# Performance work log

Measured on AMD Instinct MI355X. Metric: run time of the kernel, lower is better.

Reference implementation:

```python
import jax, jax.numpy as jnp
import numpy as np


def setup_inputs() -> dict:
    key = jax.random.key(0)
    ks = jax.random.split(key, 8)
    B, C, H, W = 8, 64, 256, 256
    Cq = C // 8
    return {
        "x": jax.random.normal(ks[0], (B, C, H, W), dtype=jnp.float32),
        "Wq": jax.random.normal(ks[1], (Cq, C), dtype=jnp.float32) * 0.1,
        "bq": jax.random.normal(ks[2], (Cq,), dtype=jnp.float32) * 0.1,
        "Wk": jax.random.normal(ks[3], (Cq, C), dtype=jnp.float32) * 0.1,
        "bk": jax.random.normal(ks[4], (Cq,), dtype=jnp.float32) * 0.1,
        "Wv": jax.random.normal(ks[5], (C, C), dtype=jnp.float32) * 0.1,
        "bv": jax.random.normal(ks[6], (C,), dtype=jnp.float32) * 0.1,
        "gamma": jax.random.normal(ks[7], (1,), dtype=jnp.float32),
    }


def _criss_cross(x, Wq, bq, Wk, bk, Wv, bv, gamma):
    # 1x1 convs == per-pixel linear maps over channel dim
    q = jnp.einsum('bchw,oc->bohw', x, Wq) + bq[None, :, None, None]  # [B,Cq,H,W]
    k = jnp.einsum('bchw,oc->bohw', x, Wk) + bk[None, :, None, None]  # [B,Cq,H,W]
    v = jnp.einsum('bchw,oc->bohw', x, Wv) + bv[None, :, None, None]  # [B,C,H,W]

    # --- column (height) attention: independent per (b, w) ---
    # attn_h[b,w,i,j] = <q[:, :, i, w], k[:, :, j, w]>, softmax over j
    attn_h = jnp.einsum('bciw,bcjw->bwij', q, k)            # [B,W,H,H]
    attn_h = jax.nn.softmax(attn_h, axis=-1)
    # torch: h_out = bmm(value[BW,C,H], attn[BW,H,H]) -> out[c,j] = sum_i v[c,i]*attn[i,j]
    h_out = jnp.einsum('bciw,bwij->bcjw', v, attn_h)        # [B,C,H,W]

    # --- row (width) attention: independent per (b, h) ---
    attn_w = jnp.einsum('bchw,bchv->bhwv', q, k)            # [B,H,W,W]
    attn_w = jax.nn.softmax(attn_w, axis=-1)
    w_out = jnp.einsum('bchw,bhwv->bchv', v, attn_w)        # [B,C,H,W]

    return gamma[0] * (h_out + w_out) + x


def reference(x, Wq, bq, Wk, bk, Wv, bv, gamma):
    return _criss_cross(x, Wq, bq, Wk, bk, Wv, bv, gamma)
```

## Files before the change

kernel.cpp:

```cpp
#include <hip/hip_runtime.h>
#include <cstddef>

namespace {

constexpr int    Bn   = 8;
constexpr int    Cc   = 64;
constexpr int    Cq   = 8;
constexpr int    Ln   = 256;
constexpr size_t HWn  = 65536;
constexpr size_t NPIX = (size_t)Bn * HWn;
constexpr size_t VPLANE = NPIX * 16;

constexpr float LOG2E = 1.44269504088896f;

constexpr size_t WT_B = 0;
constexpr size_t QH_B = 32768;
constexpr size_t QL_B = QH_B + NPIX * 8 * 2;
constexpr size_t KH_B = QL_B + NPIX * 8 * 2;
constexpr size_t KL_B = KH_B + NPIX * 8 * 2;
constexpr size_t VB_B = KL_B + NPIX * 8 * 2;
constexpr size_t HO_B = VB_B + NPIX * 64 * 2;

typedef short bf16x8 __attribute__((ext_vector_type(8)));
typedef float f32x16 __attribute__((ext_vector_type(16)));
typedef unsigned short u16x4 __attribute__((ext_vector_type(4)));

__device__ __forceinline__ unsigned short f2bf(float x) {
  union { float f; unsigned u; } c; c.f = x;
  unsigned u = c.u + 0x7FFFu + ((c.u >> 16) & 1u);
  return (unsigned short)(u >> 16);
}
__device__ __forceinline__ float bf2f(unsigned short h) {
  union { unsigned u; float f; } c; c.u = ((unsigned)h) << 16;
  return c.f;
}
__device__ __forceinline__ float fast_exp2(float x) {
#if __has_builtin(__builtin_amdgcn_exp2f)
  return __builtin_amdgcn_exp2f(x);
#else
  float r;
  asm("v_exp_f32 %0, %1" : "=v"(r) : "v"(x));
  return r;
#endif
}
__device__ __forceinline__ f32x16 zero16() {
  f32x16 z;
#pragma unroll
  for (int i = 0; i < 16; ++i) z[i] = 0.f;
  return z;
}

}

__global__ void pack_weights(const float* __restrict__ Wq,
                             const float* __restrict__ Wk,
                             const float* __restrict__ Wv,
                             float* __restrict__ wt) {
  int idx = blockIdx.x * 256 + threadIdx.x;
  if (idx >= 64 * 80) return;
  int c = idx / 80, o = idx % 80;
  float v;
  if (o < 8)       v = Wq[o * 64 + c] * LOG2E;
  else if (o < 16) v = Wk[(o - 8) * 64 + c];
  else             v = Wv[(o - 16) * 64 + c];
  wt[idx] = v;
}

__global__ __launch_bounds__(256) void qkv_kernel(
    const float* __restrict__ x, const float* __restrict__ wt,
    const float* __restrict__ bq, const float* __restrict__ bk,
    const float* __restrict__ bv,
    unsigned short* __restrict__ qh, unsigned short* __restrict__ ql,
    unsigned short* __restrict__ kh, unsigned short* __restrict__ kl,
    unsigned short* __restrict__ vb) {
  const int chunk = blockIdx.x;
  size_t p = (size_t)blockIdx.y * 256 + threadIdx.x;
  int b = (int)(p >> 16);
  int rem = (int)(p & 65535);
  const float* xb = x + (size_t)b * 64 * HWn + rem;

  float acc[16];
  if (chunk == 0) {
#pragma unroll
    for (int o = 0; o < 8; ++o) { acc[o] = bq[o] * LOG2E; acc[8 + o] = bk[o]; }
  } else {
#pragma unroll
    for (int o = 0; o < 16; ++o) acc[o] = bv[(chunk - 1) * 16 + o];
  }
  const int woff = (chunk == 0) ? 0 : 16 + (chunk - 1) * 16;

#pragma unroll 1
  for (int c0 = 0; c0 < 64; c0 += 8) {
    float xv[8];
#pragma unroll
    for (int cc = 0; cc < 8; ++cc) xv[cc] = xb[(size_t)(c0 + cc) * HWn];
#pragma unroll
    for (int cc = 0; cc < 8; ++cc) {
      const float* w = wt + (c0 + cc) * 80 + woff;
      const float xc = xv[cc];
#pragma unroll
      for (int o = 0; o < 16; ++o) acc[o] = fmaf(xc, w[o], acc[o]);
    }
  }

  if (chunk == 0) {
    unsigned h8[16], l8[16];
#pragma unroll
    for (int o = 0; o < 16; ++o) {
      h8[o] = f2bf(acc[o]);
      l8[o] = f2bf(acc[o] - bf2f((unsigned short)h8[o]));
    }
    uint4 pqh = make_uint4(h8[0] | (h8[1] << 16), h8[2] | (h8[3] << 16),
                           h8[4] | (h8[5] << 16), h8[6] | (h8[7] << 16));
    uint4 pql = make_uint4(l8[0] | (l8[1] << 16), l8[2] | (l8[3] << 16),
                           l8[4] | (l8[5] << 16), l8[6] | (l8[7] << 16));
    uint4 pkh = make_uint4(h8[8] | (h8[9] << 16), h8[10] | (h8[11] << 16),
                           h8[12] | (h8[13] << 16), h8[14] | (h8[15] << 16));
    uint4 pkl = make_uint4(l8[8] | (l8[9] << 16), l8[10] | (l8[11] << 16),
                           l8[12] | (l8[13] << 16), l8[14] | (l8[15] << 16));
    *(uint4*)(qh + p * 8) = pqh;
    *(uint4*)(ql + p * 8) = pql;
    *(uint4*)(kh + p * 8) = pkh;
    *(uint4*)(kl + p * 8) = pkl;
  } else {
    unsigned e[16];
#pragma unroll
    for (int u = 0; u < 16; ++u) e[u] = f2bf(acc[u]);
    uint4 p0 = make_uint4(e[0] | (e[1] << 16), e[2] | (e[3] << 16),
                          e[4] | (e[5] << 16), e[6] | (e[7] << 16));
    uint4 p1 = make_uint4(e[8] | (e[9] << 16), e[10] | (e[11] << 16),
                          e[12] | (e[13] << 16), e[14] | (e[15] << 16));
    unsigned short* vp = vb + (size_t)(chunk - 1) * VPLANE + p * 16;
    *(uint4*)(vp + 0) = p0;
    *(uint4*)(vp + 8) = p1;
  }
}

template <int MODE>
__global__ __launch_bounds__(256) void attn_kernel(
    const unsigned short* __restrict__ qh, const unsigned short* __restrict__ ql,
    const unsigned short* __restrict__ kh, const unsigned short* __restrict__ kl,
    const unsigned short* __restrict__ vb, float* __restrict__ o) {
  const int s = (MODE == 1) ? (((blockIdx.x & 7) << 8) | (blockIdx.x >> 3))
                            : blockIdx.x;
  const int t = threadIdx.x;
  const int b = s >> 8;
  const int r = s & 255;
  const int w = t >> 6;
  const int l = t & 63;
  const int g = l >> 5;
  const int ln = l & 31;

  __shared__ short qs_h[256 * 8], qs_l[256 * 8];
  __shared__ short ks_h[256 * 8], ks_l[256 * 8];
  __shared__ short vz[16384];
  __shared__ float Zl[256];

  size_t qkb, qk_stride;
  size_t v_pix_base, v_pix_stride;
  if (MODE == 0) {
    qkb    = (size_t)s * (Ln * Cq);  qk_stride = Cq;
    v_pix_base = (size_t)s * Ln;     v_pix_stride = 1;
  } else {
    qkb    = ((size_t)b * HWn + r) * Cq;  qk_stride = (size_t)Ln * Cq;
    v_pix_base = (size_t)b * HWn + r;     v_pix_stride = Ln;
  }

  {
    const size_t off = qkb + (size_t)t * qk_stride;
    *(bf16x8*)&qs_h[t * 8] = *(const bf16x8*)(qh + off);
    *(bf16x8*)&qs_l[t * 8] = *(const bf16x8*)(ql + off);
    *(bf16x8*)&ks_h[t * 8] = *(const bf16x8*)(kh + off);
    *(bf16x8*)&ks_l[t * 8] = *(const bf16x8*)(kl + off);
  }
  Zl[t] = 0.f;
  __syncthreads();

  {
    const short* kb = g ? ks_l : ks_h;
    bf16x8 afk0 = *(const bf16x8*)&kb[(ln + 32 * (2 * w + 0)) * 8];
    bf16x8 afk1 = *(const bf16x8*)&kb[(ln + 32 * (2 * w + 1)) * 8];
#pragma unroll 1
    for (int it = 0; it < 8; ++it) {
      int i = ln + 32 * it;
      bf16x8 bh = *(const bf16x8*)&qs_h[i * 8];
      bf16x8 bl = *(const bf16x8*)&qs_l[i * 8];
      float zp = 0.f;
      {
        f32x16 c = zero16();
        c = __builtin_amdgcn_mfma_f32_32x32x16_bf16(afk0, bh, c, 0, 0, 0);
        c = __builtin_amdgcn_mfma_f32_32x32x16_bf16(afk0, bl, c, 0, 0, 0);
#pragma unroll
        for (int rr = 0; rr < 16; ++rr) zp += fast_exp2(c[rr]);
      }
      {
        f32x16 c = zero16();
        c = __builtin_amdgcn_mfma_f32_32x32x16_bf16(afk1, bh, c, 0, 0, 0);
        c = __builtin_amdgcn_mfma_f32_32x32x16_bf16(afk1, bl, c, 0, 0, 0);
#pragma unroll
        for (int rr = 0; rr < 16; ++rr) zp += fast_exp2(c[rr]);
      }
      atomicAdd(&Zl[i], zp);
    }
  }
  __syncthreads();
  Zl[t] = 1.0f / Zl[t];
  __syncthreads();

#pragma unroll 1
  for (int rnd = 0; rnd < 16; ++rnd) {
    int idx = rnd * 256 + t;
    int i = idx >> 4;
    int c4 = (idx & 15) << 2;
    const unsigned short* vp = vb + (size_t)(c4 >> 4) * VPLANE +
                               (v_pix_base + (size_t)i * v_pix_stride) * 16 +
                               (c4 & 15);
    u16x4 raw = *(const u16x4*)vp;
    float iz = Zl[i];
    int sg = i >> 4, rem = i & 15;
    int a = rem >> 3, g2 = (rem >> 2) & 1, t0 = rem & 3;
    int e = 4 * a + t0;
#pragma unroll
    for (int u = 0; u < 4; ++u) {
      int c = c4 + u;
      int lane_s = 32 * g2 + (c & 31);
      int mt = c >> 5;
      vz[((sg * 2 + mt) * 64 + lane_s) * 8 + e] =
          (short)f2bf(bf2f(raw[u]) * iz);
    }
  }
  __syncthreads();

  f32x16 acc00 = zero16(), acc01 = zero16(), acc10 = zero16(), acc11 = zero16();
  {
    bf16x8 bkh[2], bkl[2];
#pragma unroll
    for (int nt2 = 0; nt2 < 2; ++nt2) {
      int j = ln + 32 * (2 * w + nt2);
      bkh[nt2] = *(const bf16x8*)&ks_h[j * 8];
      bkl[nt2] = *(const bf16x8*)&ks_l[j * 8];
    }
    const short* qb = g ? qs_l : qs_h;
#pragma unroll 1
    for (int it = 0; it < 8; ++it) {
      int i = ln + 32 * it;
      bf16x8 aQ = *(const bf16x8*)&qb[i * 8];
      bf16x8 pf[2][2];
#pragma unroll
      for (int nt2 = 0; nt2 < 2; ++nt2) {
        f32x16 c = zero16();
        c = __builtin_amdgcn_mfma_f32_32x32x16_bf16(aQ, bkh[nt2], c, 0, 0, 0);
        c = __builtin_amdgcn_mfma_f32_32x32x16_bf16(aQ, bkl[nt2], c, 0, 0, 0);
#pragma unroll
        for (int rr = 0; rr < 8; ++rr)
          pf[nt2][0][rr] = (short)f2bf(fast_exp2(c[rr]));
#pragma unroll
        for (int rr = 0; rr < 8; ++rr)
          pf[nt2][1][rr] = (short)f2bf(fast_exp2(c[8 + rr]));
      }
#pragma unroll
      for (int s2 = 0; s2 < 2; ++s2) {
#pragma unroll
        for (int mt = 0; mt < 2; ++mt) {
          bf16x8 vf = *(const bf16x8*)&vz[(((it * 2 + s2) * 2 + mt) * 64 + l) * 8];
          if (mt == 0) {
            acc00 = __builtin_amdgcn_mfma_f32_32x32x16_bf16(vf, pf[0][s2], acc00, 0, 0, 0);
            acc10 = __builtin_amdgcn_mfma_f32_32x32x16_bf16(vf, pf[1][s2], acc10, 0, 0, 0);
          } else {
            acc01 = __builtin_amdgcn_mfma_f32_32x32x16_bf16(vf, pf[0][s2], acc01, 0, 0, 0);
            acc11 = __builtin_amdgcn_mfma_f32_32x32x16_bf16(vf, pf[1][s2], acc11, 0, 0, 0);
          }
        }
      }
    }
  }

#pragma unroll
  for (int nt2 = 0; nt2 < 2; ++nt2) {
    int j = ln + 32 * (2 * w + nt2);
#pragma unroll
    for (int mt = 0; mt < 2; ++mt) {
      const f32x16& A = (nt2 == 0) ? (mt == 0 ? acc00 : acc01)
                                   : (mt == 0 ? acc10 : acc11);
#pragma unroll
      for (int reg = 0; reg < 16; ++reg) {
        int c = (reg & 3) + 8 * (reg >> 2) + 4 * g + 32 * mt;
        if (MODE == 0) {
          o[((size_t)b * 64 + c) * HWn + (size_t)r * 256 + j] = A[reg];
        } else {
          o[((size_t)s * 64 + c) * 256 + j] = A[reg];
        }
      }
    }
  }
}

__global__ __launch_bounds__(256) void merge_kernel(
    const float* __restrict__ wout, const float* __restrict__ ho,
    const float* __restrict__ x, const float* __restrict__ gamma,
    float* __restrict__ out) {
  const int h0 = blockIdx.x * 32;
  const int c = blockIdx.y;
  const int b = blockIdx.z;
  const int t = threadIdx.x;
  __shared__ float lds[256 * 33];

  const float g = gamma[0];

#pragma unroll
  for (int it = 0; it < 8; ++it) {
    int e = it * 256 + t;
    int w = e >> 3, q4 = (e & 7) << 2;
    float4 f = *(const float4*)&ho[(((size_t)b * 256 + w) * 64 + c) * 256 + h0 + q4];
    lds[w * 33 + q4 + 0] = f.x;
    lds[w * 33 + q4 + 1] = f.y;
    lds[w * 33 + q4 + 2] = f.z;
    lds[w * 33 + q4 + 3] = f.w;
  }
  __syncthreads();

#pragma unroll
  for (int rr = 0; rr < 32; ++rr) {
    size_t idx = (((size_t)b * 64 + c) * 256 + h0 + rr) * 256 + t;
    out[idx] = g * (wout[idx] + lds[t * 33 + rr]) + x[idx];
  }
}

extern "C" void kernel_launch(void* const* d_in, const int* in_sizes, int n_in,
                              void* d_out, int out_size, void* d_ws, size_t ws_size,
                              hipStream_t stream) {
  const float* x     = (const float*)d_in[0];
  const float* Wq    = (const float*)d_in[1];
  const float* bq    = (const float*)d_in[2];
  const float* Wk    = (const float*)d_in[3];
  const float* bk    = (const float*)d_in[4];
  const float* Wv    = (const float*)d_in[5];
  const float* bv    = (const float*)d_in[6];
  const float* gamma = (const float*)d_in[7];
  float* out = (float*)d_out;
  char*  ws  = (char*)d_ws;

  float*          wt = (float*)(ws + WT_B);
  unsigned short* qh = (unsigned short*)(ws + QH_B);
  unsigned short* ql = (unsigned short*)(ws + QL_B);
  unsigned short* kh = (unsigned short*)(ws + KH_B);
  unsigned short* kl = (unsigned short*)(ws + KL_B);
  unsigned short* vb = (unsigned short*)(ws + VB_B);
  float*          ho = (float*)(ws + HO_B);

  hipLaunchKernelGGL(pack_weights, dim3(20), dim3(256), 0, stream, Wq, Wk, Wv, wt);
  hipLaunchKernelGGL(qkv_kernel, dim3(5, 2048), dim3(256), 0, stream,
                     x, wt, bq, bk, bv, qh, ql, kh, kl, vb);
  hipLaunchKernelGGL((attn_kernel<0>), dim3(2048), dim3(256), 0, stream,
                     qh, ql, kh, kl, vb, out);
  hipLaunchKernelGGL((attn_kernel<1>), dim3(2048), dim3(256), 0, stream,
                     qh, ql, kh, kl, vb, ho);
  hipLaunchKernelGGL(merge_kernel, dim3(8, 64, 8), dim3(256), 0, stream,
                     out, ho, x, gamma, out);
}
```

Before: 557.2 us.

## Store attention partial outputs in fp16 and remap qkv grid for XCD locality

Both attention passes now write their partial outputs as fp16 into workspace buffers instead of fp32, and the merge kernel reads fp16 for both partials. This roughly halves the intermediate write and read traffic. The merge tile grows to 64 rows with an fp16 LDS transpose, and the qkv launch is flattened to a 1D grid with a block-index swizzle that groups work across XCDs. fp16 storage loses some precision in the partial sums, which could affect tolerance.

After: 504.3 us. 1.1x faster.

```diff
diff --git a/kernel.cpp b/kernel.cpp
--- a/kernel.cpp
+++ b/kernel.cpp
@@ -20,6 +20,7 @@
 constexpr size_t KL_B = KH_B + NPIX * 8 * 2;
 constexpr size_t VB_B = KL_B + NPIX * 8 * 2;
 constexpr size_t HO_B = VB_B + NPIX * 64 * 2;
+constexpr size_t WO_B = HO_B + NPIX * 64 * 2;
 
 typedef short bf16x8 __attribute__((ext_vector_type(8)));
 typedef float f32x16 __attribute__((ext_vector_type(16)));
@@ -73,8 +74,10 @@
     unsigned short* __restrict__ qh, unsigned short* __restrict__ ql,
     unsigned short* __restrict__ kh, unsigned short* __restrict__ kl,
     unsigned short* __restrict__ vb) {
-  const int chunk = blockIdx.x;
-  size_t p = (size_t)blockIdx.y * 256 + threadIdx.x;
+  const int d = blockIdx.x;
+  const int lin = (d & 7) * 1280 + (d >> 3);
+  const int chunk = lin % 5;
+  size_t p = (size_t)(lin / 5) * 256 + threadIdx.x;
   int b = (int)(p >> 16);
   int rem = (int)(p & 65535);
   const float* xb = x + (size_t)b * 64 * HWn + rem;
@@ -140,7 +143,7 @@
 __global__ __launch_bounds__(256) void attn_kernel(
     const unsigned short* __restrict__ qh, const unsigned short* __restrict__ ql,
     const unsigned short* __restrict__ kh, const unsigned short* __restrict__ kl,
-    const unsigned short* __restrict__ vb, float* __restrict__ o) {
+    const unsigned short* __restrict__ vb, _Float16* __restrict__ o) {
   const int s = (MODE == 1) ? (((blockIdx.x & 7) << 8) | (blockIdx.x >> 3))
                             : blockIdx.x;
   const int t = threadIdx.x;
@@ -286,9 +289,9 @@
       for (int reg = 0; reg < 16; ++reg) {
         int c = (reg & 3) + 8 * (reg >> 2) + 4 * g + 32 * mt;
         if (MODE == 0) {
-          o[((size_t)b * 64 + c) * HWn + (size_t)r * 256 + j] = A[reg];
+          o[((size_t)b * 64 + c) * HWn + (size_t)r * 256 + j] = (_Float16)A[reg];
         } else {
-          o[((size_t)s * 64 + c) * 256 + j] = A[reg];
+          o[((size_t)s * 64 + c) * 256 + j] = (_Float16)A[reg];
         }
       }
     }
@@ -296,33 +299,31 @@
 }
 
 __global__ __launch_bounds__(256) void merge_kernel(
-    const float* __restrict__ wout, const float* __restrict__ ho,
+    const _Float16* __restrict__ wo, const _Float16* __restrict__ ho,
     const float* __restrict__ x, const float* __restrict__ gamma,
     float* __restrict__ out) {
-  const int h0 = blockIdx.x * 32;
+  const int h0 = blockIdx.x * 64;
   const int c = blockIdx.y;
   const int b = blockIdx.z;
   const int t = threadIdx.x;
-  __shared__ float lds[256 * 33];
+  __shared__ _Float16 lds[256 * 66];
 
   const float g = gamma[0];
 
 #pragma unroll
   for (int it = 0; it < 8; ++it) {
     int e = it * 256 + t;
-    int w = e >> 3, q4 = (e & 7) << 2;
-    float4 f = *(const float4*)&ho[(((size_t)b * 256 + w) * 64 + c) * 256 + h0 + q4];
-    lds[w * 33 + q4 + 0] = f.x;
-    lds[w * 33 + q4 + 1] = f.y;
-    lds[w * 33 + q4 + 2] = f.z;
-    lds[w * 33 + q4 + 3] = f.w;
-  }
-  __syncthreads();
-
-#pragma unroll
-  for (int rr = 0; rr < 32; ++rr) {
+    int w = e >> 3, q8 = (e & 7) << 3;
+    uint4 f = *(const uint4*)&ho[(((size_t)b * 256 + w) * 64 + c) * 256 + h0 + q8];
+    unsigned* dst = (unsigned*)&lds[w * 66 + q8];
+    dst[0] = f.x; dst[1] = f.y; dst[2] = f.z; dst[3] = f.w;
+  }
+  __syncthreads();
+
+#pragma unroll 4
+  for (int rr = 0; rr < 64; ++rr) {
     size_t idx = (((size_t)b * 64 + c) * 256 + h0 + rr) * 256 + t;
-    out[idx] = g * (wout[idx] + lds[t * 33 + rr]) + x[idx];
+    out[idx] = g * ((float)wo[idx] + (float)lds[t * 66 + rr]) + x[idx];
   }
 }
 
@@ -346,15 +347,16 @@
   unsigned short* kh = (unsigned short*)(ws + KH_B);
   unsigned short* kl = (unsigned short*)(ws + KL_B);
   unsigned short* vb = (unsigned short*)(ws + VB_B);
-  float*          ho = (float*)(ws + HO_B);
+  _Float16*       ho = (_Float16*)(ws + HO_B);
+  _Float16*       wo = (_Float16*)(ws + WO_B);
 
   hipLaunchKernelGGL(pack_weights, dim3(20), dim3(256), 0, stream, Wq, Wk, Wv, wt);
-  hipLaunchKernelGGL(qkv_kernel, dim3(5, 2048), dim3(256), 0, stream,
+  hipLaunchKernelGGL(qkv_kernel, dim3(10240), dim3(256), 0, stream,
                      x, wt, bq, bk, bv, qh, ql, kh, kl, vb);
   hipLaunchKernelGGL((attn_kernel<0>), dim3(2048), dim3(256), 0, stream,
-                     qh, ql, kh, kl, vb, out);
+                     qh, ql, kh, kl, vb, wo);
   hipLaunchKernelGGL((attn_kernel<1>), dim3(2048), dim3(256), 0, stream,
                      qh, ql, kh, kl, vb, ho);
-  hipLaunchKernelGGL(merge_kernel, dim3(8, 64, 8), dim3(256), 0, stream,
-                     out, ho, x, gamma, out);
-}
+  hipLaunchKernelGGL(merge_kernel, dim3(4, 64, 8), dim3(256), 0, stream,
+                     wo, ho, x, gamma, out);
+}
```
